# Performance work log

Hardware: AMD Instinct MI355X
Metric: run time of the kernel (lower is better)

The kernel has to match this reference:

```python
import jax, jax.numpy as jnp
from jax import lax
import numpy as np

K = 3
IMG = 512
BATCH = 32


def setup_inputs() -> dict:
    key = jax.random.key(0)
    k1, k2, k3 = jax.random.split(key, 3)
    x = jax.random.normal(k1, (BATCH, 1, IMG, IMG), dtype=jnp.float32)
    # Conv2d(1, K*K, K) weight/bias, torch default init scale ~ 1/sqrt(fan_in)
    fan_in = 1 * K * K
    bound = 1.0 / np.sqrt(fan_in)
    W = jax.random.uniform(k2, (K * K, 1, K, K), dtype=jnp.float32, minval=-bound, maxval=bound)
    b = jax.random.uniform(k3, (K * K,), dtype=jnp.float32, minval=-bound, maxval=bound)
    return {"x": x, "W": W, "b": b}


def reference(x, W, b):
    k = W.shape[-1]
    pad = k // 2                      # k_radius
    P = x.shape[-1] + k - 1           # padded/self.img_size spatial size
    # x_tmp = F.pad(x, pad on all sides); firstConv = Conv2d(1, k^2, k, padding=pad)(x_tmp)
    x_tmp = jnp.pad(x, ((0, 0), (0, 0), (pad, pad), (pad, pad)))
    fc = lax.conv_general_dilated(
        x_tmp, W, window_strides=(1, 1), padding=[(pad, pad), (pad, pad)],
        dimension_numbers=("NCHW", "OIHW", "NCHW"),
    ) + b[None, :, None, None]        # (B, k^2, P, P)
    t = jnp.tanh(fc)
    # F.pad(x, (k-1-i, i, k-1-j, j)) == xp[:, :, j:j+P, i:i+P] with xp padded by k-1 everywhere
    xp = jnp.pad(x, ((0, 0), (0, 0), (k - 1, k - 1), (k - 1, k - 1)))
    out = jnp.zeros((x.shape[0], 1, P, P), dtype=x.dtype)
    for i in range(k):                # small fixed k^2 loop over kernel taps
        for j in range(k):
            out = out + xp[:, :, j:j + P, i:i + P] * t[:, k * i + j][:, None]
    return out[:, :, pad:-pad, pad:-pad]
```

## Files before the change

kernel.cpp:

```cpp
#include <hip/hip_runtime.h>
#include <stdint.h>

#define IMG  512
#define CPT  8
#define CGRP (IMG / CPT)

typedef _Float16 h2    __attribute__((ext_vector_type(2)));
typedef __fp16   f16x2 __attribute__((ext_vector_type(2)));

static __device__ __forceinline__ h2 pkrtz(float a, float b) {
    f16x2 t = __builtin_amdgcn_cvt_pkrtz(a, b);
    return __builtin_bit_cast(h2, t);
}

#if __has_builtin(__builtin_amdgcn_fdot2)
#define FDOT2(a, b, c) __builtin_amdgcn_fdot2((a), (b), (c), false)
#else
static __device__ __forceinline__ float fdot2_sw(h2 a, h2 b, float c) {
    return fmaf((float)a.x, (float)b.x, fmaf((float)a.y, (float)b.y, c));
}
#define FDOT2(a, b, c) fdot2_sw((a), (b), (c))
#endif


__global__ __launch_bounds__(256) void fused_convtap_kernel(
    const float* __restrict__ x,
    const float* __restrict__ W,
    const float* __restrict__ Bv,
    float* __restrict__ out)
{
    __shared__ float lut[2048];

    const int tid = blockIdx.x * 256 + threadIdx.x;
    const int xg  = tid & (CGRP - 1);
    const int row = tid >> 6;
    const int y   = row & (IMG - 1);
    const int x0  = xg * CPT;

    const float* xr = x + (size_t)row * IMG;
    const bool has_l = (x0 > 0);
    const bool has_r = (x0 < IMG - CPT);

    float r0[10], r1[10], r2[10];
    {
        auto load_row = [&](const float* p, float (&r)[10]) {
            float4 a = *reinterpret_cast<const float4*>(p + x0);
            float4 c = *reinterpret_cast<const float4*>(p + x0 + 4);
            r[1] = a.x; r[2] = a.y; r[3] = a.z; r[4] = a.w;
            r[5] = c.x; r[6] = c.y; r[7] = c.z; r[8] = c.w;
            r[0] = has_l ? p[x0 - 1] : 0.0f;
            r[9] = has_r ? p[x0 + 8] : 0.0f;
        };
        auto zero_row = [&](float (&r)[10]) {
#pragma unroll
            for (int k = 0; k < 10; ++k) r[k] = 0.0f;
        };
        if (y > 0)       load_row(xr - IMG, r0); else zero_row(r0);
                         load_row(xr,       r1);
        if (y < IMG - 1) load_row(xr + IMG, r2); else zero_row(r2);
    }

    {
        const float E2 = 7.38905609893065f;
        const float xi0 = fmaf((float)threadIdx.x, 0.00390625f,
                               0.001953125f - 4.0f);
        float e = __builtin_amdgcn_exp2f(xi0 * 2.8853900817779268f);
#pragma unroll
        for (int k = 0; k < 8; ++k) {
            lut[threadIdx.x + (k << 8)] =
                1.0f - 2.0f * __builtin_amdgcn_rcpf(e + 1.0f);
            e *= E2;
        }
    }
    __syncthreads();

    h2 u[9][4];
    float w8[9], bv[9];
#pragma unroll
    for (int c = 0; c < 9; ++c) {
#pragma unroll
        for (int k = 0; k < 4; ++k)
            u[c][k] = pkrtz(W[c * 9 + 2 * k], W[c * 9 + 2 * k + 1]);
        w8[c] = W[c * 9 + 8];
        bv[c] = Bv[c];
    }

    auto tlu = [&](float v) -> float {
        float t = __builtin_amdgcn_fmed3f(fmaf(v, 256.0f, 1024.0f),
                                          0.0f, 2047.0f);
        return lut[(int)t];
    };

    float o[CPT];
#pragma unroll
    for (int tp = 0; tp < 4; ++tp) {
        const int t0 = 2 * tp;
        h2 A0 = pkrtz(r0[t0],     r0[t0 + 1]);
        h2 B0 = pkrtz(r0[t0 + 2], r1[t0]);
        h2 C0 = pkrtz(r1[t0 + 1], r1[t0 + 2]);
        h2 D0 = pkrtz(r2[t0],     r2[t0 + 1]);
        h2 A1 = pkrtz(r0[t0 + 1], r0[t0 + 2]);
        h2 B1 = pkrtz(r0[t0 + 3], r1[t0 + 1]);
        h2 C1 = pkrtz(r1[t0 + 2], r1[t0 + 3]);
        h2 D1 = pkrtz(r2[t0 + 1], r2[t0 + 2]);

        float ox = 0.0f, oy = 0.0f;
#pragma unroll
        for (int c = 0; c < 9; ++c) {
            float fx = bv[c], fy = bv[c];
            fx = FDOT2(A0, u[c][0], fx);
            fy = FDOT2(A1, u[c][0], fy);
            fx = FDOT2(B0, u[c][1], fx);
            fy = FDOT2(B1, u[c][1], fy);
            fx = FDOT2(C0, u[c][2], fx);
            fy = FDOT2(C1, u[c][2], fy);
            fx = FDOT2(D0, u[c][3], fx);
            fy = FDOT2(D1, u[c][3], fy);
            fx = fmaf(r2[t0 + 2], w8[c], fx);
            fy = fmaf(r2[t0 + 3], w8[c], fy);

            const float thx = tlu(fx);
            const float thy = tlu(fy);

            const int i = c / 3, j = c - 3 * i;
            const float* rj = (j == 0) ? r0 : (j == 1) ? r1 : r2;
            ox = fmaf(rj[t0 + i],     thx, ox);
            oy = fmaf(rj[t0 + 1 + i], thy, oy);
        }
        o[t0] = ox; o[t0 + 1] = oy;
    }

    float* orow = out + (size_t)row * IMG + x0;
    *reinterpret_cast<float4*>(orow)     = make_float4(o[0], o[1], o[2], o[3]);
    *reinterpret_cast<float4*>(orow + 4) = make_float4(o[4], o[5], o[6], o[7]);
}

extern "C" void kernel_launch(void* const* d_in, const int* in_sizes, int n_in,
                              void* d_out, int out_size, void* d_ws, size_t ws_size,
                              hipStream_t stream) {
    const float* x  = (const float*)d_in[0];
    const float* W  = (const float*)d_in[1];
    const float* Bv = (const float*)d_in[2];
    float* out = (float*)d_out;

    const int batch   = in_sizes[0] / (IMG * IMG);
    const int threads = batch * IMG * CGRP;
    const int grid    = threads / 256;
    fused_convtap_kernel<<<grid, 256, 0, stream>>>(x, W, Bv, out);
}
```

Baseline: 34.79 us.

## Compute two output rows per thread and prepack weights in a separate kernel

Each thread now produces a 2x8 output tile, loading four input rows instead of three for one row, which cuts redundant global row loads and halves the grid. The tanh LUT build and weight setup are amortized over twice the outputs per block. A tiny prepack kernel converts the weights to packed fp16 and stores them in workspace, so the main kernel reads ready-made values. This adds an extra kernel launch, raises register pressure, and halves the number of threads, which may reduce occupancy and latency hiding.

New measurement: 38.36 us. 1.1x slower.

```diff
diff --git a/kernel.cpp b/kernel.cpp
--- a/kernel.cpp
+++ b/kernel.cpp
@@ -22,26 +22,91 @@
 #define FDOT2(a, b, c) fdot2_sw((a), (b), (c))
 #endif
 
+__global__ void prepack_kernel(const float* __restrict__ W,
+                               const float* __restrict__ B,
+                               uint32_t* __restrict__ ws) {
+    int c = threadIdx.x;
+    if (c < 9) {
+        const float* wc = W + c * 9;
+#pragma unroll
+        for (int k = 0; k < 4; ++k) {
+            h2 t = pkrtz(wc[2 * k], wc[2 * k + 1]);
+            ws[c * 4 + k] = __builtin_bit_cast(uint32_t, t);
+        }
+        ((float*)ws)[36 + c] = wc[8];
+        ((float*)ws)[45 + c] = B[c];
+    }
+}
+
+__device__ __forceinline__ void compute8(
+    const float (&r0)[10], const float (&r1)[10], const float (&r2)[10],
+    const uint32_t (&uu)[9][4], const float (&w8)[9], const float (&bv)[9],
+    const float (&lut)[2048], float (&o)[8])
+{
+    auto tlu = [&](float v) -> float {
+        float t = __builtin_amdgcn_fmed3f(fmaf(v, 256.0f, 1024.0f),
+                                          0.0f, 2047.0f);
+        return lut[(int)t];
+    };
+#pragma unroll
+    for (int tp = 0; tp < 4; ++tp) {
+        const int t0 = 2 * tp;
+        h2 A0 = pkrtz(r0[t0],     r0[t0 + 1]);
+        h2 B0 = pkrtz(r0[t0 + 2], r1[t0]);
+        h2 C0 = pkrtz(r1[t0 + 1], r1[t0 + 2]);
+        h2 D0 = pkrtz(r2[t0],     r2[t0 + 1]);
+        h2 A1 = pkrtz(r0[t0 + 1], r0[t0 + 2]);
+        h2 B1 = pkrtz(r0[t0 + 3], r1[t0 + 1]);
+        h2 C1 = pkrtz(r1[t0 + 2], r1[t0 + 3]);
+        h2 D1 = pkrtz(r2[t0 + 1], r2[t0 + 2]);
+
+        float ox = 0.0f, oy = 0.0f;
+#pragma unroll
+        for (int c = 0; c < 9; ++c) {
+            float fx = bv[c], fy = bv[c];
+            fx = FDOT2(A0, __builtin_bit_cast(h2, uu[c][0]), fx);
+            fy = FDOT2(A1, __builtin_bit_cast(h2, uu[c][0]), fy);
+            fx = FDOT2(B0, __builtin_bit_cast(h2, uu[c][1]), fx);
+            fy = FDOT2(B1, __builtin_bit_cast(h2, uu[c][1]), fy);
+            fx = FDOT2(C0, __builtin_bit_cast(h2, uu[c][2]), fx);
+            fy = FDOT2(C1, __builtin_bit_cast(h2, uu[c][2]), fy);
+            fx = FDOT2(D0, __builtin_bit_cast(h2, uu[c][3]), fx);
+            fy = FDOT2(D1, __builtin_bit_cast(h2, uu[c][3]), fy);
+            fx = fmaf(r2[t0 + 2], w8[c], fx);
+            fy = fmaf(r2[t0 + 3], w8[c], fy);
+
+            const float thx = tlu(fx);
+            const float thy = tlu(fy);
+
+            const int i = c / 3, j = c - 3 * i;
+            const float* rj = (j == 0) ? r0 : (j == 1) ? r1 : r2;
+            ox = fmaf(rj[t0 + i],     thx, ox);
+            oy = fmaf(rj[t0 + 1 + i], thy, oy);
+        }
+        o[t0] = ox; o[t0 + 1] = oy;
+    }
+}
 
 __global__ __launch_bounds__(256) void fused_convtap_kernel(
     const float* __restrict__ x,
-    const float* __restrict__ W,
-    const float* __restrict__ Bv,
+    const uint32_t* __restrict__ wsu,
     float* __restrict__ out)
 {
     __shared__ float lut[2048];
 
     const int tid = blockIdx.x * 256 + threadIdx.x;
     const int xg  = tid & (CGRP - 1);
-    const int row = tid >> 6;
-    const int y   = row & (IMG - 1);
+    const int rp  = tid >> 6;
+    const int y0  = (rp & 255) << 1;
+    const int b   = rp >> 8;
     const int x0  = xg * CPT;
+    const int rowbase = (b << 9) + y0;
 
-    const float* xr = x + (size_t)row * IMG;
+    const float* xr = x + (size_t)rowbase * IMG;
     const bool has_l = (x0 > 0);
     const bool has_r = (x0 < IMG - CPT);
 
-    float r0[10], r1[10], r2[10];
+    float r0[10], r1[10], r2[10], r3[10];
     {
         auto load_row = [&](const float* p, float (&r)[10]) {
             float4 a = *reinterpret_cast<const float4*>(p + x0);
@@ -55,9 +120,10 @@
 #pragma unroll
             for (int k = 0; k < 10; ++k) r[k] = 0.0f;
         };
-        if (y > 0)       load_row(xr - IMG, r0); else zero_row(r0);
-                         load_row(xr,       r1);
-        if (y < IMG - 1) load_row(xr + IMG, r2); else zero_row(r2);
+        if (y0 > 0)        load_row(xr - IMG,     r0); else zero_row(r0);
+                           load_row(xr,           r1);
+                           load_row(xr + IMG,     r2);
+        if (y0 < IMG - 2)  load_row(xr + 2 * IMG, r3); else zero_row(r3);
     }
 
     {
@@ -74,65 +140,27 @@
     }
     __syncthreads();
 
-    h2 u[9][4];
-    float w8[9], bv[9];
+    uint32_t uu[9][4];
 #pragma unroll
-    for (int c = 0; c < 9; ++c) {
+    for (int c = 0; c < 9; ++c)
 #pragma unroll
         for (int k = 0; k < 4; ++k)
-            u[c][k] = pkrtz(W[c * 9 + 2 * k], W[c * 9 + 2 * k + 1]);
-        w8[c] = W[c * 9 + 8];
-        bv[c] = Bv[c];
-    }
+            uu[c][k] = wsu[c * 4 + k];
+    float w8[9], bv[9];
+    const float* w8v = (const float*)(wsu + 36);
+    const float* bvv = (const float*)(wsu + 45);
+#pragma unroll
+    for (int c = 0; c < 9; ++c) { w8[c] = w8v[c]; bv[c] = bvv[c]; }
 
-    auto tlu = [&](float v) -> float {
-        float t = __builtin_amdgcn_fmed3f(fmaf(v, 256.0f, 1024.0f),
-                                          0.0f, 2047.0f);
-        return lut[(int)t];
-    };
+    float oA[8], oB[8];
+    compute8(r0, r1, r2, uu, w8, bv, lut, oA);
+    compute8(r1, r2, r3, uu, w8, bv, lut, oB);
 
-    float o[CPT];
-#pragma unroll
-    for (int tp = 0; tp < 4; ++tp) {
-        const int t0 = 2 * tp;
-        h2 A0 = pkrtz(r0[t0],     r0[t0 + 1]);
-        h2 B0 = pkrtz(r0[t0 + 2], r1[t0]);
-        h2 C0 = pkrtz(r1[t0 + 1], r1[t0 + 2]);
-        h2 D0 = pkrtz(r2[t0],     r2[t0 + 1]);
-        h2 A1 = pkrtz(r0[t0 + 1], r0[t0 + 2]);
-        h2 B1 = pkrtz(r0[t0 + 3], r1[t0 + 1]);
-        h2 C1 = pkrtz(r1[t0 + 2], r1[t0 + 3]);
-        h2 D1 = pkrtz(r2[t0 + 1], r2[t0 + 2]);
-
-        float ox = 0.0f, oy = 0.0f;
-#pragma unroll
-        for (int c = 0; c < 9; ++c) {
-            float fx = bv[c], fy = bv[c];
-            fx = FDOT2(A0, u[c][0], fx);
-            fy = FDOT2(A1, u[c][0], fy);
-            fx = FDOT2(B0, u[c][1], fx);
-            fy = FDOT2(B1, u[c][1], fy);
-            fx = FDOT2(C0, u[c][2], fx);
-            fy = FDOT2(C1, u[c][2], fy);
-            fx = FDOT2(D0, u[c][3], fx);
-            fy = FDOT2(D1, u[c][3], fy);
-            fx = fmaf(r2[t0 + 2], w8[c], fx);
-            fy = fmaf(r2[t0 + 3], w8[c], fy);
-
-            const float thx = tlu(fx);
-            const float thy = tlu(fy);
-
-            const int i = c / 3, j = c - 3 * i;
-            const float* rj = (j == 0) ? r0 : (j == 1) ? r1 : r2;
-            ox = fmaf(rj[t0 + i],     thx, ox);
-            oy = fmaf(rj[t0 + 1 + i], thy, oy);
-        }
-        o[t0] = ox; o[t0 + 1] = oy;
-    }
-
-    float* orow = out + (size_t)row * IMG + x0;
-    *reinterpret_cast<float4*>(orow)     = make_float4(o[0], o[1], o[2], o[3]);
-    *reinterpret_cast<float4*>(orow + 4) = make_float4(o[4], o[5], o[6], o[7]);
+    float* orow = out + (size_t)rowbase * IMG + x0;
+    *reinterpret_cast<float4*>(orow)           = make_float4(oA[0], oA[1], oA[2], oA[3]);
+    *reinterpret_cast<float4*>(orow + 4)       = make_float4(oA[4], oA[5], oA[6], oA[7]);
+    *reinterpret_cast<float4*>(orow + IMG)     = make_float4(oB[0], oB[1], oB[2], oB[3]);
+    *reinterpret_cast<float4*>(orow + IMG + 4) = make_float4(oB[4], oB[5], oB[6], oB[7]);
 }
 
 extern "C" void kernel_launch(void* const* d_in, const int* in_sizes, int n_in,
@@ -142,9 +170,12 @@
     const float* W  = (const float*)d_in[1];
     const float* Bv = (const float*)d_in[2];
     float* out = (float*)d_out;
+    uint32_t* ws = (uint32_t*)d_ws;
+
+    prepack_kernel<<<1, 64, 0, stream>>>(W, Bv, ws);
 
     const int batch   = in_sizes[0] / (IMG * IMG);
-    const int threads = batch * IMG * CGRP;
+    const int threads = batch * (IMG / 2) * CGRP;
     const int grid    = threads / 256;
-    fused_convtap_kernel<<<grid, 256, 0, stream>>>(x, W, Bv, out);
+    fused_convtap_kernel<<<grid, 256, 0, stream>>>(x, ws, out);
 }
```
